# Kernel optimization log

Measured on AMD Instinct MI355X. Metric: run time of the kernel, lower is better.

## Reference

```python
import math
import jax, jax.numpy as jnp
import numpy as np

B, T_BI, D_BI = 64, 3000, 128
T_SW, D_SW = 375, 192
T_S1, D_S1 = 188, 192
N_FIRES = 300          # static fire count (target_lengths all = 300 -> beta = 1, ceil(sum)=300)
D_MODEL = 512
SCALE = 4.0            # scale_factor
EPS_LN = 1e-5


def _cif_integrate(h, alpha, thr, n_fires):
    """Vectorized CIF: cumsum + two scatter-adds (matches torch _cif_forward).
    h [B,T,D], alpha [B,T], thr [B,1] -> [B,n_fires,D]."""
    Bq, T, D = h.shape
    a = alpha / thr                       # normalize so boundaries sit at integers
    c = jnp.cumsum(a, axis=1)
    prev = c - a
    kp = jnp.floor(prev)
    kc = jnp.floor(c)
    fired = kc > kp                       # frame crosses a token boundary
    w_hi = jnp.where(fired, (c - kc) * thr, 0.0)          # leftover into new token
    w_lo = jnp.where(fired, (kp + 1.0 - prev) * thr, alpha)  # portion completing old token
    ip = jnp.clip(kp.astype(jnp.int32), 0, n_fires - 1)
    ic = jnp.clip(kc.astype(jnp.int32), 0, n_fires - 1)
    bidx = jnp.broadcast_to(jnp.arange(Bq)[:, None], (Bq, T))
    out = jnp.zeros((Bq, n_fires, D), h.dtype)
    out = out.at[bidx, ip].add(w_lo[..., None] * h)
    out = out.at[bidx, ic].add(w_hi[..., None] * h)
    return out


def _interp(src, t_cont, t_bi):
    """Linear interp of src [B,Ts,D] at continuous fire times t_cont [B,N] (given on the T_bi grid)."""
    Bq, Ts, D = src.shape
    t = t_cont * Ts / t_bi
    lo = jnp.clip(t.astype(jnp.int32), 0, Ts - 2)
    w = (t - lo.astype(t.dtype))[..., None]
    idx_lo = jnp.broadcast_to(lo[..., None], (Bq, t.shape[1], D))
    g_lo = jnp.take_along_axis(src, idx_lo, axis=1)
    g_hi = jnp.take_along_axis(src, idx_lo + 1, axis=1)
    return (1.0 - w) * g_lo + w * g_hi


def _forward(fire_signal, acoustic_src, acoustic_src_s1, conv_w, ln_g, ln_b, wp_w, wp_b,
             film_s0_w, film_s0_b, film_s1_w, film_s1_b, tproj_w, tproj_b,
             aproj_w, aproj_b, bproj_w, bproj_b, target_lengths):
    Bq, T_bi, _ = fire_signal.shape
    # 1) weight predictor: depthwise conv (k=1, no bias) -> LN -> Linear -> sigmoid
    x = fire_signal * conv_w                                   # depthwise 1x1 conv
    mu = jnp.mean(x, axis=-1, keepdims=True)
    var = jnp.var(x, axis=-1, keepdims=True)
    xn = (x - mu) * jax.lax.rsqrt(var + EPS_LN) * ln_g + ln_b
    alpha = SCALE * jax.nn.sigmoid(xn @ wp_w + wp_b)           # [B,T]
    tgt = target_lengths.astype(alpha.dtype)
    qty_loss = jnp.mean(jnp.abs(jnp.sum(alpha, axis=1) - tgt))
    # training-mode alpha normalization (sum alpha_cif == target)
    sum_a = jnp.clip(jnp.sum(alpha, axis=1, keepdims=True), 1e-8)
    alpha_cif = alpha * (tgt[:, None] / sum_a)
    # dynamic threshold beta = sum / ceil(sum)  (== 1 here since targets are integers)
    sum_cif = jnp.sum(alpha_cif, axis=1)
    ceil_sum = jax.lax.stop_gradient(jnp.clip(jnp.ceil(sum_cif), 1.0))
    thr = (sum_cif / ceil_sum)[:, None]                        # [B,1]
    # 2) CIF integration of temporal channel
    acoustic_temporal = _cif_integrate(fire_signal, alpha_cif, thr, N_FIRES)  # [B,N,128]
    # continuous fire times
    cum = jnp.cumsum(alpha_cif, axis=1)
    thresholds = jnp.arange(1, N_FIRES + 1, dtype=alpha.dtype)[None, :] * thr  # [B,N]
    ff = jax.vmap(jnp.searchsorted)(cum, thresholds)
    ff = jnp.minimum(ff, T_bi - 1)
    t_lo = jnp.maximum(ff - 1, 0)
    cum_at = jnp.take_along_axis(cum, t_lo, axis=1)
    a_at = jnp.take_along_axis(alpha_cif, ff, axis=1)
    t_cont = t_lo.astype(alpha.dtype) + (thresholds - cum_at) / jnp.clip(a_at, 1e-8)
    t_cont = jnp.clip(t_cont, 0.0, T_bi - 1)
    # 3) S0 pitch channel: interp + FiLM
    acoustic_pitch = _interp(acoustic_src, t_cont, T_bi)       # [B,N,192]
    film0 = acoustic_temporal @ film_s0_w + film_s0_b
    g0, b0 = jnp.split(film0, 2, axis=-1)
    pitch_mod = g0 * acoustic_pitch + b0
    # 4) project + combine
    embs = (acoustic_temporal @ tproj_w + tproj_b) + (pitch_mod @ aproj_w + aproj_b)
    # S1 beat channel
    acoustic_beat = _interp(acoustic_src_s1, t_cont, T_bi)     # [B,N,192]
    film1 = acoustic_temporal @ film_s1_w + film_s1_b
    g1, b1 = jnp.split(film1, 2, axis=-1)
    beat_mod = g1 * acoustic_beat + b1
    embs = embs + (beat_mod @ bproj_w + bproj_b)
    return embs, alpha, qty_loss


def setup_inputs() -> dict:
    key = jax.random.key(0)
    ks = jax.random.split(key, 14)
    # weight_proj bias init per module: alpha_init = target_fires/encoder_len
    p = min((128.0 / 3000.0) / SCALE, 0.99)
    wp_bias = math.log(p / (1.0 - p))
    f32 = jnp.float32
    return {
        "fire_signal": jax.random.normal(ks[0], (B, T_BI, D_BI), f32),
        "acoustic_src": jax.random.normal(ks[1], (B, T_SW, D_SW), f32),
        "acoustic_src_s1": jax.random.normal(ks[2], (B, T_S1, D_S1), f32),
        "target_lengths": jnp.full((B,), N_FIRES, jnp.int32),
        "conv_w": 1.0 + 0.1 * jax.random.normal(ks[3], (D_BI,), f32),
        "ln_g": jnp.ones((D_BI,), f32),
        "ln_b": jnp.zeros((D_BI,), f32),
        "wp_w": 0.02 * jax.random.normal(ks[4], (D_BI,), f32),
        "wp_b": jnp.asarray(wp_bias, f32),
        "film_s0_w": 0.02 * jax.random.normal(ks[5], (D_BI, 2 * D_SW), f32),
        "film_s0_b": jnp.concatenate([jnp.ones((D_SW,), f32), jnp.zeros((D_SW,), f32)]),
        "film_s1_w": 0.02 * jax.random.normal(ks[6], (D_BI, 2 * D_S1), f32),
        "film_s1_b": jnp.concatenate([jnp.ones((D_S1,), f32), jnp.zeros((D_S1,), f32)]),
        "tproj_w": 0.02 * jax.random.normal(ks[7], (D_BI, D_MODEL), f32),
        "tproj_b": jnp.zeros((D_MODEL,), f32),
        "aproj_w": 0.02 * jax.random.normal(ks[8], (D_SW, D_MODEL), f32),
        "aproj_b": jnp.zeros((D_MODEL,), f32),
        "bproj_w": 0.02 * jax.random.normal(ks[9], (D_S1, D_MODEL), f32),
        "bproj_b": jnp.zeros((D_MODEL,), f32),
    }


def reference(fire_signal, acoustic_src, acoustic_src_s1, target_lengths, conv_w, ln_g, ln_b,
              wp_w, wp_b, film_s0_w, film_s0_b, film_s1_w, film_s1_b, tproj_w, tproj_b,
              aproj_w, aproj_b, bproj_w, bproj_b):
    return _forward(fire_signal, acoustic_src, acoustic_src_s1, conv_w, ln_g, ln_b, wp_w, wp_b,
                    film_s0_w, film_s0_b, film_s1_w, film_s1_b, tproj_w, tproj_b,
                    aproj_w, aproj_b, bproj_w, bproj_b, target_lengths)
```

## Files before the change

### kernel.cpp

```cpp
#include <hip/hip_runtime.h>
#include <math.h>

#define BQ 64
#define TBI 3000
#define DBI 128
#define TSW 375
#define TS1 188
#define DSW 192
#define NF 300
#define DMODEL 512
#define EPSLN 1e-5f

typedef __bf16 bf16x8 __attribute__((ext_vector_type(8)));
typedef float f32x4 __attribute__((ext_vector_type(4)));

__device__ __forceinline__ unsigned short f2bf(float f) {
    unsigned u = __float_as_uint(f);
    unsigned r = (u + 0x7FFFu + ((u >> 16) & 1u)) >> 16;
    return (unsigned short)r;
}

#define ALPHA_BLOCKS 24000

__global__ __launch_bounds__(256) void k_alpha_prep(
    const float* __restrict__ fs, const float* __restrict__ conv_w,
    const float* __restrict__ ln_g, const float* __restrict__ ln_b,
    const float* __restrict__ wp_w, const float* __restrict__ wp_b,
    float* __restrict__ alpha_out,
    const float* __restrict__ f0w, const float* __restrict__ f1w,
    const float* __restrict__ tw, const float* __restrict__ aw, const float* __restrict__ bw,
    const float* __restrict__ f0b, const float* __restrict__ f1b,
    const float* __restrict__ tb, const float* __restrict__ apb, const float* __restrict__ bpb,
    unsigned short* __restrict__ Wg, unsigned short* __restrict__ Wb,
    unsigned short* __restrict__ W2,
    float* __restrict__ gbias, float* __restrict__ bbias, float* __restrict__ bias2,
    float* __restrict__ qtyo)
{
    if (blockIdx.x >= ALPHA_BLOCKS) {
        int pbid = blockIdx.x - ALPHA_BLOCKS;
        if (pbid == 1216) {
            for (int c = threadIdx.x; c < 512; c += 256) {
                if (c < 384) {
                    gbias[c] = c < 192 ? f0b[c] : f1b[c - 192];
                    bbias[c] = c < 192 ? f0b[c + 192] : f1b[c - 192 + 192];
                }
                bias2[c] = tb[c] + apb[c] + bpb[c];
            }
            if (threadIdx.x == 0) qtyo[0] = 0.f;
            return;
        }
        int i = pbid * 256 + threadIdx.x;
        if (i < 49152) {
            int j = i & 7, lane = (i >> 3) & 63, kt = (i >> 9) & 3, nt = i >> 11;
            int k = kt * 32 + (lane >> 4) * 8 + j;
            int n = nt * 16 + (lane & 15);
            float g, b;
            if (n < 192) { g = f0w[k * 384 + n];         b = f0w[k * 384 + n + 192]; }
            else         { g = f1w[k * 384 + (n - 192)]; b = f1w[k * 384 + (n - 192) + 192]; }
            Wg[i] = f2bf(g); Wb[i] = f2bf(b);
        } else {
            int ii = i - 49152;
            int j = ii & 7, lane = (ii >> 3) & 63, kt = (ii >> 9) & 15, nt = ii >> 13;
            int k = kt * 32 + (lane >> 4) * 8 + j;
            int n = nt * 16 + (lane & 15);
            float v;
            if (k < 128)      v = tw[k * 512 + n];
            else if (k < 320) v = aw[(k - 128) * 512 + n];
            else              v = bw[(k - 320) * 512 + n];
            W2[ii] = f2bf(v);
        }
        return;
    }
    int wave = threadIdx.x >> 6, lane = threadIdx.x & 63;
    int l = lane & 31;
    long g = (long)blockIdx.x * 8 + wave * 2 + (lane >> 5);
    const float* row = fs + g * DBI;
    float4 f  = *(const float4*)&row[4 * l];
    float4 cw = *(const float4*)&conv_w[4 * l];
    float4 x; x.x = f.x * cw.x; x.y = f.y * cw.y; x.z = f.z * cw.z; x.w = f.w * cw.w;
    float s = x.x + x.y + x.z + x.w;
    for (int m = 16; m >= 1; m >>= 1) s += __shfl_xor(s, m, 64);
    float mu = s * (1.0f / 128.0f);
    float4 d; d.x = x.x - mu; d.y = x.y - mu; d.z = x.z - mu; d.w = x.w - mu;
    float q = d.x * d.x + d.y * d.y + d.z * d.z + d.w * d.w;
    for (int m = 16; m >= 1; m >>= 1) q += __shfl_xor(q, m, 64);
    float var = q * (1.0f / 128.0f);
    float rs = rsqrtf(var + EPSLN);
    float4 lg = *(const float4*)&ln_g[4 * l];
    float4 lb = *(const float4*)&ln_b[4 * l];
    float4 wp = *(const float4*)&wp_w[4 * l];
    float z = (d.x * rs * lg.x + lb.x) * wp.x + (d.y * rs * lg.y + lb.y) * wp.y
            + (d.z * rs * lg.z + lb.z) * wp.z + (d.w * rs * lg.w + lb.w) * wp.w;
    for (int m = 16; m >= 1; m >>= 1) z += __shfl_xor(z, m, 64);
    z += wp_b[0];
    float a = 4.0f / (1.0f + expf(-z));
    if (l == 0) alpha_out[g] = a;
}

__global__ __launch_bounds__(1024) void k_scan4(
    const float* __restrict__ alpha, const int* __restrict__ tlen,
    float2* __restrict__ params, float* __restrict__ qtyo,
    float2* __restrict__ c2, float* __restrict__ tcont, int* __restrict__ ffout)
{
    __shared__ float2 sc[TBI];
    __shared__ float2 part[2][1024];
    __shared__ double wpart[16];
    int b = blockIdx.x, tid = threadIdx.x;
    int wv = tid >> 6, ln = tid & 63;
    const float* ar = alpha + (long)b * TBI;
    double s = 0.0;
    for (int t = tid; t < TBI; t += 1024) s += (double)ar[t];
    for (int m = 32; m >= 1; m >>= 1) s += __shfl_xor(s, m, 64);
    if (ln == 0) wpart[wv] = s;
    __syncthreads();
    if (wv == 0) {
        double d = (ln < 16) ? wpart[ln] : 0.0;
        for (int m = 8; m >= 1; m >>= 1) d += __shfl_xor(d, m, 64);
        if (ln == 0) wpart[0] = d;
    }
    __syncthreads();
    double sum_a = wpart[0];
    __syncthreads();
    double tgt = (double)tlen[b];
    double sa = sum_a < 1e-8 ? 1e-8 : sum_a;
    float r = (float)(tgt / sa);
    double s2 = 0.0;
    for (int t = tid; t < TBI; t += 1024) s2 += (double)(ar[t] * r);
    for (int m = 32; m >= 1; m >>= 1) s2 += __shfl_xor(s2, m, 64);
    if (ln == 0) wpart[wv] = s2;
    __syncthreads();
    if (wv == 0) {
        double d = (ln < 16) ? wpart[ln] : 0.0;
        for (int m = 8; m >= 1; m >>= 1) d += __shfl_xor(d, m, 64);
        if (ln == 0) wpart[0] = d;
    }
    __syncthreads();
    float sum_cif = (float)wpart[0];
    float cs = ceilf(sum_cif); if (cs < 1.0f) cs = 1.0f;
    float thr = sum_cif / cs;
    float rthr = 1.0f / thr;
    if (tid == 0) {
        params[b] = make_float2(r, thr);
        atomicAdd(qtyo, (float)fabs(sum_a - tgt) * (1.0f / (float)BQ));
    }
    int base = tid * 3;
    float2 run = make_float2(0.f, 0.f);
    if (base < TBI) {
        for (int j = 0; j < 3; ++j) {
            int t = base + j;
            float ac = ar[t] * r;
            run.x += ac * rthr; run.y += ac;
            sc[t] = run;
        }
    }
    part[0][tid] = (base < TBI) ? run : make_float2(0.f, 0.f);
    __syncthreads();
    int srcb = 0;
    for (int d = 1; d < 1024; d <<= 1) {
        float2 v = part[srcb][tid];
        if (tid >= d) { float2 u = part[srcb][tid - d]; v.x += u.x; v.y += u.y; }
        part[srcb ^ 1][tid] = v;
        srcb ^= 1;
        __syncthreads();
    }
    if (base < TBI && tid > 0) {
        float2 off = part[srcb][tid - 1];
        for (int j = 0; j < 3; ++j) { sc[base + j].x += off.x; sc[base + j].y += off.y; }
    }
    __syncthreads();
    for (int t = tid; t < TBI; t += 1024) {
        float ac = ar[t] * r;
        c2[(long)b * TBI + t] = make_float2(sc[t].x, ac);
    }
    if (tid < NF) {
        float v = (float)(tid + 1) * thr;
        int lo = 0, hi = TBI;
        while (lo < hi) { int mid = (lo + hi) >> 1; if (sc[mid].y < v) lo = mid + 1; else hi = mid; }
        int ff = lo; if (ff > TBI - 1) ff = TBI - 1;
        ffout[b * NF + tid] = ff;
        int tl = ff - 1; if (tl < 0) tl = 0;
        float cum_at = sc[tl].y;
        float a_at = ar[ff] * r;
        if (a_at < 1e-8f) a_at = 1e-8f;
        float tc = (float)tl + (v - cum_at) / a_at;
        tc = fminf(fmaxf(tc, 0.0f), (float)(TBI - 1));
        tcont[b * NF + tid] = tc;
    }
}

__global__ __launch_bounds__(256) void k_cif4(
    const float* __restrict__ fs, const float2* __restrict__ c2,
    const int* __restrict__ ffA, const float2* __restrict__ params,
    unsigned short* __restrict__ at)
{
    int wid = threadIdx.x >> 6, lane = threadIdx.x & 63;
    int wg = blockIdx.x * 4 + wid;
    int b = wg / NF, j = wg - b * NF;
    const int* ffb = ffA + b * NF;
    int s = (j == 0) ? 0 : ffb[j - 1];
    int e = (j == NF - 1) ? (TBI - 1) : ffb[j];
    float thr = params[b].y;
    float rthr = 1.0f / thr;
    const float2* cb = c2 + (long)b * TBI;
    const float* fb = fs + (long)b * TBI * DBI;
    float a0 = 0.f, a1 = 0.f;
    for (int t = s; t <= e; ++t) {
        float2 v = cb[t];
        float2 h = *(const float2*)&fb[(long)t * DBI + 2 * lane];
        float c = v.x, ac = v.y;
        float av = ac * rthr;
        float prev = c - av;
        float kp = floorf(prev), kc = floorf(c);
        bool fired = kc > kp;
        float w_lo = fired ? (kp + 1.0f - prev) * thr : ac;
        float w_hi = fired ? (c - kc) * thr : 0.0f;
        int ip = (int)kp; if (ip > NF - 1) ip = NF - 1; if (ip < 0) ip = 0;
        int ic = (int)kc; if (ic > NF - 1) ic = NF - 1; if (ic < 0) ic = 0;
        if (ip == j) { a0 += w_lo * h.x; a1 += w_lo * h.y; }
        if (fired && ic == j) { a0 += w_hi * h.x; a1 += w_hi * h.y; }
    }
    unsigned short* ab = at + (long)b * NF * DBI;
    *(unsigned*)&ab[j * DBI + 2 * lane] = (unsigned)f2bf(a0) | ((unsigned)f2bf(a1) << 16);
}

#define EROWS 64
__global__ __launch_bounds__(512, 4) void k_emb7(
    const unsigned short* __restrict__ atb, const float* __restrict__ tcont,
    const float* __restrict__ src0, const float* __restrict__ src1,
    const unsigned short* __restrict__ Wg, const unsigned short* __restrict__ Wb,
    const unsigned short* __restrict__ W2,
    const float* __restrict__ gbias, const float* __restrict__ bbias,
    const float* __restrict__ bias2, float* __restrict__ embs)
{
    __shared__ __align__(16) unsigned short X[EROWS][520];
    __shared__ float s_w0[EROWS], s_w1[EROWS];
    __shared__ int s_lo0[EROWS], s_lo1[EROWS], s_b[EROWS];
    int tid = threadIdx.x;
    int wave = tid >> 6, lane = tid & 63;
    long r0 = (long)blockIdx.x * EROWS;
    for (int idx = tid; idx < 1024; idx += 512) {
        int r = idx >> 4, k8 = (idx & 15) * 8;
        *(uint4*)&X[r][k8] = *(const uint4*)&atb[(r0 + r) * DBI + k8];
    }
    if (tid < EROWS) {
        long g = r0 + tid;
        s_b[tid] = (int)(g / NF);
        float tc = tcont[g];
        float t0 = tc * ((float)TSW / 3000.0f);
        int lo0 = (int)t0; if (lo0 > TSW - 2) lo0 = TSW - 2; if (lo0 < 0) lo0 = 0;
        s_lo0[tid] = lo0; s_w0[tid] = t0 - (float)lo0;
        float t1 = tc * ((float)TS1 / 3000.0f);
        int lo1 = (int)t1; if (lo1 > TS1 - 2) lo1 = TS1 - 2; if (lo1 < 0) lo1 = 0;
        s_lo1[tid] = lo1; s_w1[tid] = t1 - (float)lo1;
    }
    __syncthreads();
    int mrow = lane & 15, quad = lane >> 4;
    for (int nt = wave; nt < 24; nt += 8) {
        f32x4 ag[4], av[4];
        #pragma unroll
        for (int m = 0; m < 4; ++m) { ag[m] = (f32x4){0,0,0,0}; av[m] = (f32x4){0,0,0,0}; }
        #pragma unroll
        for (int kt = 0; kt < 4; ++kt) {
            bf16x8 bg = *(const bf16x8*)&Wg[(((nt * 4 + kt) * 64) + lane) * 8];
            bf16x8 bb = *(const bf16x8*)&Wb[(((nt * 4 + kt) * 64) + lane) * 8];
            #pragma unroll
            for (int m = 0; m < 4; ++m) {
                bf16x8 a = *(const bf16x8*)&X[mrow + 16 * m][kt * 32 + quad * 8];
                ag[m] = __builtin_amdgcn_mfma_f32_16x16x32_bf16(a, bg, ag[m], 0, 0, 0);
                av[m] = __builtin_amdgcn_mfma_f32_16x16x32_bf16(a, bb, av[m], 0, 0, 0);
            }
        }
        int c = nt * 16 + mrow;
        bool sel = c >= DSW;
        int cc = sel ? c - DSW : c;
        const float* S = sel ? src1 : src0;
        int Ts = sel ? TS1 : TSW;
        float gb = gbias[c], bbv = bbias[c];
        #pragma unroll
        for (int m = 0; m < 4; ++m) {
            #pragma unroll
            for (int q = 0; q < 4; ++q) {
                int r = 16 * m + quad * 4 + q;
                int b = s_b[r];
                int lo = sel ? s_lo1[r] : s_lo0[r];
                float w = sel ? s_w1[r] : s_w0[r];
                const float* Sp = S + ((long)b * Ts + lo) * DSW + cc;
                float pv = (1.0f - w) * Sp[0] + w * Sp[DSW];
                X[r][128 + c] = f2bf((ag[m][q] + gb) * pv + (av[m][q] + bbv));
            }
        }
    }
    __syncthreads();
    f32x4 acc[4][4];
    #pragma unroll
    for (int m = 0; m < 4; ++m)
        #pragma unroll
        for (int n = 0; n < 4; ++n) acc[m][n] = (f32x4){0, 0, 0, 0};
    for (int kt = 0; kt < 16; ++kt) {
        bf16x8 a[4];
        #pragma unroll
        for (int m = 0; m < 4; ++m) a[m] = *(const bf16x8*)&X[mrow + 16 * m][kt * 32 + quad * 8];
        #pragma unroll
        for (int n = 0; n < 4; ++n) {
            int nt = wave * 4 + n;
            bf16x8 bfv = *(const bf16x8*)&W2[((nt * 16 + kt) * 64 + lane) * 8];
            #pragma unroll
            for (int m = 0; m < 4; ++m)
                acc[m][n] = __builtin_amdgcn_mfma_f32_16x16x32_bf16(a[m], bfv, acc[m][n], 0, 0, 0);
        }
    }
    #pragma unroll
    for (int n = 0; n < 4; ++n) {
        int cbase = (wave * 4 + n) * 16 + mrow;
        float bv = bias2[cbase];
        #pragma unroll
        for (int m = 0; m < 4; ++m)
            #pragma unroll
            for (int q = 0; q < 4; ++q)
                embs[(r0 + 16 * m + quad * 4 + q) * DMODEL + cbase] = acc[m][n][q] + bv;
    }
}

extern "C" void kernel_launch(void* const* d_in, const int* in_sizes, int n_in,
                              void* d_out, int out_size, void* d_ws, size_t ws_size,
                              hipStream_t stream)
{
    const float* fs     = (const float*)d_in[0];
    const float* src0   = (const float*)d_in[1];
    const float* src1   = (const float*)d_in[2];
    const int*   tlen   = (const int*)d_in[3];
    const float* conv_w = (const float*)d_in[4];
    const float* ln_g   = (const float*)d_in[5];
    const float* ln_b   = (const float*)d_in[6];
    const float* wp_w   = (const float*)d_in[7];
    const float* wp_b   = (const float*)d_in[8];
    const float* f0w    = (const float*)d_in[9];
    const float* f0b    = (const float*)d_in[10];
    const float* f1w    = (const float*)d_in[11];
    const float* f1b    = (const float*)d_in[12];
    const float* tw     = (const float*)d_in[13];
    const float* tb     = (const float*)d_in[14];
    const float* aw     = (const float*)d_in[15];
    const float* apb    = (const float*)d_in[16];
    const float* bw     = (const float*)d_in[17];
    const float* bpb    = (const float*)d_in[18];

    float* embs  = (float*)d_out;
    float* alpha = embs + (long)BQ * NF * DMODEL;
    float* qtyo  = alpha + (long)BQ * TBI;

    char* ws = (char*)d_ws;
    size_t off = 0;
    unsigned short* at = (unsigned short*)(ws + off); off += 4915200;
    float2* c2     = (float2*)(ws + off); off += 1536000;
    float*  tcont  = (float*)(ws + off);  off += 76800;
    int*    ffA    = (int*)(ws + off);    off += 76800;
    float2* params = (float2*)(ws + off); off += 512;
    unsigned short* Wg = (unsigned short*)(ws + off); off += 98304;
    unsigned short* Wb = (unsigned short*)(ws + off); off += 98304;
    unsigned short* W2 = (unsigned short*)(ws + off); off += 524288;
    float* gbias = (float*)(ws + off); off += 1536;
    float* bbias = (float*)(ws + off); off += 1536;
    float* bias2 = (float*)(ws + off); off += 2048;

    k_alpha_prep<<<ALPHA_BLOCKS + 1217, 256, 0, stream>>>(
        fs, conv_w, ln_g, ln_b, wp_w, wp_b, alpha,
        f0w, f1w, tw, aw, bw, f0b, f1b, tb, apb, bpb,
        Wg, Wb, W2, gbias, bbias, bias2, qtyo);
    k_scan4<<<BQ, 1024, 0, stream>>>(alpha, tlen, params, qtyo, c2, tcont, ffA);
    k_cif4<<<(BQ * NF) / 4, 256, 0, stream>>>(fs, c2, ffA, params, at);
    k_emb7<<<(BQ * NF) / EROWS, 512, 0, stream>>>(at, tcont, src0, src1,
                                                  Wg, Wb, W2, gbias, bbias, bias2, embs);
}
```

Baseline: 286.0 us.

## Halve emb tile rows, prefetch interpolation gathers, unroll CIF loop by two

The embedding kernel now processes 32 rows per block instead of 64, which doubles the block count and raises parallelism across the GPU. Before the FiLM GEMM it gathers all interpolation source values into registers, so global latency can overlap with the MFMA work. The CIF integration loop is unrolled by two to expose more memory-level parallelism. The costs are twice as many blocks, each reloading the Wg/Wb/W2 weights, and higher register pressure from the prefetch arrays.

Result: faster. 264.6 us (-7.5%).

```diff
diff --git a/kernel.cpp b/kernel.cpp
--- a/kernel.cpp
+++ b/kernel.cpp
@@ -188,7 +188,7 @@
     }
 }
 
-__global__ __launch_bounds__(256) void k_cif4(
+__global__ __launch_bounds__(256) void k_cif5(
     const float* __restrict__ fs, const float2* __restrict__ c2,
     const int* __restrict__ ffA, const float2* __restrict__ params,
     unsigned short* __restrict__ at)
@@ -204,27 +204,31 @@
     const float2* cb = c2 + (long)b * TBI;
     const float* fb = fs + (long)b * TBI * DBI;
     float a0 = 0.f, a1 = 0.f;
-    for (int t = s; t <= e; ++t) {
-        float2 v = cb[t];
-        float2 h = *(const float2*)&fb[(long)t * DBI + 2 * lane];
-        float c = v.x, ac = v.y;
-        float av = ac * rthr;
-        float prev = c - av;
-        float kp = floorf(prev), kc = floorf(c);
-        bool fired = kc > kp;
-        float w_lo = fired ? (kp + 1.0f - prev) * thr : ac;
-        float w_hi = fired ? (c - kc) * thr : 0.0f;
-        int ip = (int)kp; if (ip > NF - 1) ip = NF - 1; if (ip < 0) ip = 0;
-        int ic = (int)kc; if (ic > NF - 1) ic = NF - 1; if (ic < 0) ic = 0;
-        if (ip == j) { a0 += w_lo * h.x; a1 += w_lo * h.y; }
-        if (fired && ic == j) { a0 += w_hi * h.x; a1 += w_hi * h.y; }
-    }
+    #define CIF_BODY(T) do { \
+        float2 v = cb[T]; \
+        float2 h = *(const float2*)&fb[(long)(T) * DBI + 2 * lane]; \
+        float c = v.x, ac = v.y; \
+        float av = ac * rthr; \
+        float prev = c - av; \
+        float kp = floorf(prev), kc = floorf(c); \
+        bool fired = kc > kp; \
+        float w_lo = fired ? (kp + 1.0f - prev) * thr : ac; \
+        float w_hi = fired ? (c - kc) * thr : 0.0f; \
+        int ip = (int)kp; if (ip > NF - 1) ip = NF - 1; if (ip < 0) ip = 0; \
+        int ic = (int)kc; if (ic > NF - 1) ic = NF - 1; if (ic < 0) ic = 0; \
+        if (ip == j) { a0 += w_lo * h.x; a1 += w_lo * h.y; } \
+        if (fired && ic == j) { a0 += w_hi * h.x; a1 += w_hi * h.y; } \
+    } while (0)
+    int t = s;
+    for (; t + 1 <= e; t += 2) { CIF_BODY(t); CIF_BODY(t + 1); }
+    if (t <= e) CIF_BODY(t);
+    #undef CIF_BODY
     unsigned short* ab = at + (long)b * NF * DBI;
     *(unsigned*)&ab[j * DBI + 2 * lane] = (unsigned)f2bf(a0) | ((unsigned)f2bf(a1) << 16);
 }
 
-#define EROWS 64
-__global__ __launch_bounds__(512, 4) void k_emb7(
+#define EROWS 32
+__global__ __launch_bounds__(512, 4) void k_emb8(
     const unsigned short* __restrict__ atb, const float* __restrict__ tcont,
     const float* __restrict__ src0, const float* __restrict__ src1,
     const unsigned short* __restrict__ Wg, const unsigned short* __restrict__ Wb,
@@ -238,8 +242,8 @@
     int tid = threadIdx.x;
     int wave = tid >> 6, lane = tid & 63;
     long r0 = (long)blockIdx.x * EROWS;
-    for (int idx = tid; idx < 1024; idx += 512) {
-        int r = idx >> 4, k8 = (idx & 15) * 8;
+    {
+        int r = tid >> 4, k8 = (tid & 15) * 8;
         *(uint4*)&X[r][k8] = *(const uint4*)&atb[(r0 + r) * DBI + k8];
     }
     if (tid < EROWS) {
@@ -255,58 +259,80 @@
     }
     __syncthreads();
     int mrow = lane & 15, quad = lane >> 4;
-    for (int nt = wave; nt < 24; nt += 8) {
-        f32x4 ag[4], av[4];
-        #pragma unroll
-        for (int m = 0; m < 4; ++m) { ag[m] = (f32x4){0,0,0,0}; av[m] = (f32x4){0,0,0,0}; }
-        #pragma unroll
-        for (int kt = 0; kt < 4; ++kt) {
-            bf16x8 bg = *(const bf16x8*)&Wg[(((nt * 4 + kt) * 64) + lane) * 8];
-            bf16x8 bb = *(const bf16x8*)&Wb[(((nt * 4 + kt) * 64) + lane) * 8];
-            #pragma unroll
-            for (int m = 0; m < 4; ++m) {
-                bf16x8 a = *(const bf16x8*)&X[mrow + 16 * m][kt * 32 + quad * 8];
-                ag[m] = __builtin_amdgcn_mfma_f32_16x16x32_bf16(a, bg, ag[m], 0, 0, 0);
-                av[m] = __builtin_amdgcn_mfma_f32_16x16x32_bf16(a, bb, av[m], 0, 0, 0);
-            }
-        }
+    float v0[3][2][4], v1[3][2][4], wgt[3][2][4];
+    float gbv[3], bbv_[3];
+    #pragma unroll
+    for (int i = 0; i < 3; ++i) {
+        int nt = wave + 8 * i;
         int c = nt * 16 + mrow;
         bool sel = c >= DSW;
         int cc = sel ? c - DSW : c;
         const float* S = sel ? src1 : src0;
         int Ts = sel ? TS1 : TSW;
-        float gb = gbias[c], bbv = bbias[c];
-        #pragma unroll
-        for (int m = 0; m < 4; ++m) {
+        gbv[i] = gbias[c]; bbv_[i] = bbias[c];
+        #pragma unroll
+        for (int m = 0; m < 2; ++m) {
             #pragma unroll
             for (int q = 0; q < 4; ++q) {
                 int r = 16 * m + quad * 4 + q;
-                int b = s_b[r];
+                int bb = s_b[r];
                 int lo = sel ? s_lo1[r] : s_lo0[r];
                 float w = sel ? s_w1[r] : s_w0[r];
-                const float* Sp = S + ((long)b * Ts + lo) * DSW + cc;
-                float pv = (1.0f - w) * Sp[0] + w * Sp[DSW];
-                X[r][128 + c] = f2bf((ag[m][q] + gb) * pv + (av[m][q] + bbv));
+                const float* Sp = S + ((long)bb * Ts + lo) * DSW + cc;
+                v0[i][m][q] = Sp[0];
+                v1[i][m][q] = Sp[DSW];
+                wgt[i][m][q] = w;
             }
         }
     }
-    __syncthreads();
-    f32x4 acc[4][4];
     #pragma unroll
-    for (int m = 0; m < 4; ++m)
-        #pragma unroll
-        for (int n = 0; n < 4; ++n) acc[m][n] = (f32x4){0, 0, 0, 0};
+    for (int i = 0; i < 3; ++i) {
+        int nt = wave + 8 * i;
+        f32x4 ag0 = {0,0,0,0}, ab0 = {0,0,0,0}, ag1 = {0,0,0,0}, ab1 = {0,0,0,0};
+        #pragma unroll
+        for (int kt = 0; kt < 4; ++kt) {
+            bf16x8 a0 = *(const bf16x8*)&X[mrow][kt * 32 + quad * 8];
+            bf16x8 a1 = *(const bf16x8*)&X[mrow + 16][kt * 32 + quad * 8];
+            bf16x8 bg = *(const bf16x8*)&Wg[(((nt * 4 + kt) * 64) + lane) * 8];
+            bf16x8 bb = *(const bf16x8*)&Wb[(((nt * 4 + kt) * 64) + lane) * 8];
+            ag0 = __builtin_amdgcn_mfma_f32_16x16x32_bf16(a0, bg, ag0, 0, 0, 0);
+            ab0 = __builtin_amdgcn_mfma_f32_16x16x32_bf16(a0, bb, ab0, 0, 0, 0);
+            ag1 = __builtin_amdgcn_mfma_f32_16x16x32_bf16(a1, bg, ag1, 0, 0, 0);
+            ab1 = __builtin_amdgcn_mfma_f32_16x16x32_bf16(a1, bb, ab1, 0, 0, 0);
+        }
+        int c = nt * 16 + mrow;
+        float gb = gbv[i], bbv = bbv_[i];
+        #pragma unroll
+        for (int q = 0; q < 4; ++q) {
+            {
+                int r = quad * 4 + q;
+                float w = wgt[i][0][q];
+                float pv = (1.0f - w) * v0[i][0][q] + w * v1[i][0][q];
+                X[r][128 + c] = f2bf((ag0[q] + gb) * pv + (ab0[q] + bbv));
+            }
+            {
+                int r = quad * 4 + q + 16;
+                float w = wgt[i][1][q];
+                float pv = (1.0f - w) * v0[i][1][q] + w * v1[i][1][q];
+                X[r][128 + c] = f2bf((ag1[q] + gb) * pv + (ab1[q] + bbv));
+            }
+        }
+    }
+    __syncthreads();
+    f32x4 acc[2][4];
+    #pragma unroll
+    for (int h = 0; h < 2; ++h)
+        #pragma unroll
+        for (int n = 0; n < 4; ++n) acc[h][n] = (f32x4){0, 0, 0, 0};
     for (int kt = 0; kt < 16; ++kt) {
-        bf16x8 a[4];
-        #pragma unroll
-        for (int m = 0; m < 4; ++m) a[m] = *(const bf16x8*)&X[mrow + 16 * m][kt * 32 + quad * 8];
+        bf16x8 a0 = *(const bf16x8*)&X[mrow][kt * 32 + quad * 8];
+        bf16x8 a1 = *(const bf16x8*)&X[mrow + 16][kt * 32 + quad * 8];
         #pragma unroll
         for (int n = 0; n < 4; ++n) {
             int nt = wave * 4 + n;
             bf16x8 bfv = *(const bf16x8*)&W2[((nt * 16 + kt) * 64 + lane) * 8];
-            #pragma unroll
-            for (int m = 0; m < 4; ++m)
-                acc[m][n] = __builtin_amdgcn_mfma_f32_16x16x32_bf16(a[m], bfv, acc[m][n], 0, 0, 0);
+            acc[0][n] = __builtin_amdgcn_mfma_f32_16x16x32_bf16(a0, bfv, acc[0][n], 0, 0, 0);
+            acc[1][n] = __builtin_amdgcn_mfma_f32_16x16x32_bf16(a1, bfv, acc[1][n], 0, 0, 0);
         }
     }
     #pragma unroll
@@ -314,10 +340,10 @@
         int cbase = (wave * 4 + n) * 16 + mrow;
         float bv = bias2[cbase];
         #pragma unroll
-        for (int m = 0; m < 4; ++m)
-            #pragma unroll
-            for (int q = 0; q < 4; ++q)
-                embs[(r0 + 16 * m + quad * 4 + q) * DMODEL + cbase] = acc[m][n][q] + bv;
+        for (int q = 0; q < 4; ++q) {
+            embs[(r0 + quad * 4 + q) * DMODEL + cbase] = acc[0][n][q] + bv;
+            embs[(r0 + 16 + quad * 4 + q) * DMODEL + cbase] = acc[1][n][q] + bv;
+        }
     }
 }
 
@@ -368,7 +394,7 @@
         f0w, f1w, tw, aw, bw, f0b, f1b, tb, apb, bpb,
         Wg, Wb, W2, gbias, bbias, bias2, qtyo);
     k_scan4<<<BQ, 1024, 0, stream>>>(alpha, tlen, params, qtyo, c2, tcont, ffA);
-    k_cif4<<<(BQ * NF) / 4, 256, 0, stream>>>(fs, c2, ffA, params, at);
-    k_emb7<<<(BQ * NF) / EROWS, 512, 0, stream>>>(at, tcont, src0, src1,
+    k_cif5<<<(BQ * NF) / 4, 256, 0, stream>>>(fs, c2, ffA, params, at);
+    k_emb8<<<(BQ * NF) / EROWS, 512, 0, stream>>>(at, tcont, src0, src1,
                                                   Wg, Wb, W2, gbias, bbias, bias2, embs);
 }
```
